# Performance work log

Hardware: AMD Instinct MI355X
Metric: run time of the kernel (lower is better)

The kernel has to match this reference:

```python
import jax, jax.numpy as jnp
import numpy as np

N_NODES = 5000
N_EDGES = 50000
HIDDEN = 64
EDGE_DIM = 16


def setup_inputs() -> dict:
    key = jax.random.key(0)
    ks = jax.random.split(key, 8)
    d = HIDDEN
    h = jax.random.normal(ks[0], (N_NODES, d), dtype=jnp.float32)
    edge_index = jax.random.randint(ks[1], (2, N_EDGES), 0, N_NODES, dtype=jnp.int64)
    edge_features = jax.random.normal(ks[2], (N_EDGES, EDGE_DIM), dtype=jnp.float32)
    # edge-network MLP: Linear(edge_dim, d) -> ReLU -> Linear(d, d*d)
    W1 = jax.random.normal(ks[3], (EDGE_DIM, d), dtype=jnp.float32) * (1.0 / np.sqrt(EDGE_DIM))
    b1 = jnp.zeros((d,), dtype=jnp.float32)
    W2 = jax.random.normal(ks[4], (d, d * d), dtype=jnp.float32) * (1.0 / np.sqrt(d))
    b2 = jnp.zeros((d * d,), dtype=jnp.float32)
    # GRUCell params (torch layout: rows = [reset; update; new])
    W_ih = jax.random.normal(ks[5], (3 * d, d), dtype=jnp.float32) * (1.0 / np.sqrt(d))
    W_hh = jax.random.normal(ks[6], (3 * d, d), dtype=jnp.float32) * (1.0 / np.sqrt(d))
    b_ih = jnp.zeros((3 * d,), dtype=jnp.float32)
    b_hh = jnp.zeros((3 * d,), dtype=jnp.float32)
    return {"h": h, "edge_index": edge_index, "edge_features": edge_features,
            "W1": W1, "b1": b1, "W2": W2, "b2": b2,
            "W_ih": W_ih, "W_hh": W_hh, "b_ih": b_ih, "b_hh": b_hh}


def reference(h, edge_index, edge_features, W1, b1, W2, b2, W_ih, W_hh, b_ih, b_hh):
    n_nodes, d = h.shape
    src, tgt = edge_index[0], edge_index[1]
    # 1) gather sender states
    h_w = h[src]  # (E, d)
    # 2-3) edge MLP -> per-edge transformation matrices (E, d, d)
    A = jax.nn.relu(edge_features @ W1 + b1) @ W2 + b2
    A = A.reshape(-1, d, d)
    # 4) per-edge matvec messages
    msg = jnp.einsum('eij,ej->ei', A, h_w)  # (E, d)
    # 5) scatter-sum aggregation per target node
    m = jax.ops.segment_sum(msg, tgt, num_segments=n_nodes)  # (N, d)
    # 6) GRUCell(m, h) - torch semantics
    gi = m @ W_ih.T + b_ih   # (N, 3d)
    gh = h @ W_hh.T + b_hh   # (N, 3d)
    i_r, i_z, i_n = jnp.split(gi, 3, axis=-1)
    h_r, h_z, h_n = jnp.split(gh, 3, axis=-1)
    r = jax.nn.sigmoid(i_r + h_r)
    z = jax.nn.sigmoid(i_z + h_z)
    n = jnp.tanh(i_n + r * h_n)
    h_new = (1.0 - z) * n + z * h
    return h_new
```

## Files before the change

### kernel.cpp

```cpp
#include <hip/hip_runtime.h>
#include <math.h>

#define N_NODES 5000
#define N_EDGES 50000
#define POISON_I ((int)0xAAAAAAAAu)

typedef _Float16 f16x8 __attribute__((ext_vector_type(8)));
typedef _Float16 f16x4 __attribute__((ext_vector_type(4)));
typedef _Float16 f16x2 __attribute__((ext_vector_type(2)));
typedef float    f32x4 __attribute__((ext_vector_type(4)));

static __device__ __forceinline__ f32x4 mfma16f(f16x8 a, f16x8 b, f32x4 c) {
    return __builtin_amdgcn_mfma_f32_16x16x32_f16(a, b, c, 0, 0, 0);
}
static __device__ __forceinline__ f32x4 mfma16k16(f16x4 a, f16x4 b, f32x4 c) {
    return __builtin_amdgcn_mfma_f32_16x16x16f16(a, b, c, 0, 0, 0);
}

__global__ void prep_kernel(const float* __restrict__ W2, const float* __restrict__ b2,
                            const float* __restrict__ Wih, const float* __restrict__ Whh,
                            const int* __restrict__ ei,
                            _Float16* __restrict__ Br, _Float16* __restrict__ Bg2,
                            int* __restrict__ cnt) {
    int g = blockIdx.x * 256 + threadIdx.x;
    if (g < 33792) {
        int nt = g / 8448, rem = g - nt * 8448;
        int ks = rem >> 6, lane = rem & 63;
        int lo = lane & 15, q = lane >> 4;
        int i = nt * 16 + lo, kap0 = ks * 32 + q * 8;
        f16x8 v;
#pragma unroll
        for (int p = 0; p < 8; ++p) {
            int kap = kap0 + p;
            int k2 = kap >> 7, rem2 = kap & 127;
            int j = rem2 >> 1, k = k2 * 2 + (rem2 & 1);
            float x = 0.f;
            if (k < 64) x = W2[(size_t)k * 4096 + i * 64 + j];
            else if (k == 64) x = b2[i * 64 + j];
            v[p] = (_Float16)x;
        }
        *(f16x8*)(Br + (size_t)g * 8) = v;
        return;
    }
    g -= 33792;
    if (g < 3072) {
        int ct = g >> 7, ks = (g >> 6) & 1, lane = g & 63;
        int lo = lane & 15, q = lane >> 4;
        const float* src = (ct < 12) ? Wih : Whh;
        int r = ((ct < 12) ? ct : ct - 12) * 16 + lo;
        int j0 = ks * 32 + q * 8;
        f16x8 v;
#pragma unroll
        for (int p = 0; p < 8; ++p) v[p] = (_Float16)src[r * 64 + j0 + p];
        *(f16x8*)(Bg2 + (size_t)g * 8) = v;
        return;
    }
    g -= 3072;
    if (g < N_EDGES) atomicAdd(&cnt[ei[N_EDGES + g]], 1);
}

__global__ __launch_bounds__(1024) void scan_kernel(const int* __restrict__ cnt,
                                                    int* __restrict__ off,
                                                    int* __restrict__ cur) {
    __shared__ int s[1024];
    int tid = threadIdx.x;
    int base = tid * 5;
    int loc[5]; int sum = 0;
#pragma unroll
    for (int q = 0; q < 5; ++q) {
        int v = (base + q < N_NODES) ? (cnt[base + q] - POISON_I) : 0;
        loc[q] = sum; sum += v;
    }
    s[tid] = sum; __syncthreads();
    for (int d = 1; d < 1024; d <<= 1) {
        int v = (tid >= d) ? s[tid - d] : 0;
        __syncthreads();
        s[tid] += v;
        __syncthreads();
    }
    int excl = (tid > 0) ? s[tid - 1] : 0;
#pragma unroll
    for (int q = 0; q < 5; ++q)
        if (base + q < N_NODES) { off[base + q] = excl + loc[q]; cur[base + q] = excl + loc[q]; }
    if (tid == 1023) off[N_NODES] = excl + sum;
}

__global__ void scatter_kernel(const int* __restrict__ ei, int* __restrict__ cur,
                               int* __restrict__ srcp, int* __restrict__ eidp) {
    int e = blockIdx.x * 256 + threadIdx.x;
    if (e < N_EDGES) {
        int q = atomicAdd(&cur[ei[N_EDGES + e]], 1);
        srcp[q] = ei[e];
        eidp[q] = e;
    }
}

__global__ __launch_bounds__(1024, 4) void fused_gnn(
    const int* __restrict__ toff, const int* __restrict__ srcp,
    const int* __restrict__ eidp, const float* __restrict__ ef,
    const float* __restrict__ W1, const float* __restrict__ b1,
    const float* __restrict__ h, const _Float16* __restrict__ Br,
    const _Float16* __restrict__ Bg2, const float* __restrict__ bih,
    const float* __restrict__ bhh, float* __restrict__ out)
{
    extern __shared__ __align__(16) char smem[];
    _Float16* tS  = (_Float16*)(smem);
    _Float16* hHi = (_Float16*)(smem + 33280);
    _Float16* hLo = (_Float16*)(smem + 66560);
    int*      nsl = (int*)(smem + 99840);
    _Float16* As    = (_Float16*)(smem);
    float*    mbuf  = (float*)(smem + 33024);
    _Float16* mls   = (_Float16*)(smem + 33024 + 12480);
    _Float16* hls16 = (_Float16*)(smem + 33024 + 14784);
    float*    gbuf  = (float*)(smem + 33024 + 17088);

    int tid = threadIdx.x, w16 = tid >> 6, lane = tid & 63;
    int lo = lane & 15, q = lane >> 4;
    int nt = w16 & 3, kq = w16 >> 2;
    int m0 = blockIdx.x * 16;

    if (tid < 17) {
        int nn = m0 + tid; if (nn > N_NODES) nn = N_NODES;
        nsl[tid] = toff[nn];
    }
    float w1c[16];
#pragma unroll
    for (int k = 0; k < 16; ++k) w1c[k] = W1[k * 64 + lane];
    float b1l = b1[lane];

    f32x4 z4 = {0.f, 0.f, 0.f, 0.f};
    f32x4 acc[4][4];
#pragma unroll
    for (int a = 0; a < 4; ++a)
#pragma unroll
        for (int b = 0; b < 4; ++b) acc[a][b] = z4;
    float sacc = 0.f;
    __syncthreads();

    int nwin = 0;
    {
        int mx = 0;
#pragma unroll
        for (int n = 0; n < 16; ++n) {
            int c = nsl[n + 1] - nsl[n];
            if (c > mx) mx = c;
        }
        nwin = (mx + 15) >> 4;
    }

    for (int ws = 0; ws < nwin; ++ws) {
        if (ws) __syncthreads();
        int epos = ws * 16 + w16;
#pragma unroll 4
        for (int r = 0; r < 16; ++r) {
            int base = nsl[r], cnt2 = nsl[r + 1] - base;
            int cc = r * 16 + w16;
            if (epos < cnt2) {
                int ge = __builtin_amdgcn_readfirstlane(base + epos);
                int src = srcp[ge], eid = eidp[ge];
                float hv = h[(size_t)src * 64 + lane];
                _Float16 hh = (_Float16)hv;
                _Float16 hl = (_Float16)(hv - (float)hh);
                const float* efr = ef + (size_t)eid * 16;
                float tacc = b1l;
#pragma unroll
                for (int k = 0; k < 16; ++k) tacc += efr[k] * w1c[k];
                tS [lane * 260 + cc] = (_Float16)fmaxf(tacc, 0.f);
                hHi[lane * 260 + cc] = hh;
                hLo[lane * 260 + cc] = hl;
            } else {
                tS [lane * 260 + cc] = (_Float16)0.f;
                hHi[lane * 260 + cc] = (_Float16)0.f;
                hLo[lane * 260 + cc] = (_Float16)0.f;
            }
        }
        __syncthreads();
        int cb = w16 * 16 + q * 4;
        f16x4 at[4];
#pragma unroll
        for (int mi = 0; mi < 4; ++mi)
            at[mi] = *(const f16x4*)&tS[(mi * 16 + lo) * 260 + cb];
#pragma unroll
        for (int ni = 0; ni < 4; ++ni) {
            f16x4 bh = *(const f16x4*)&hHi[(ni * 16 + lo) * 260 + cb];
            f16x4 bl = *(const f16x4*)&hLo[(ni * 16 + lo) * 260 + cb];
#pragma unroll
            for (int mi = 0; mi < 4; ++mi) {
                acc[mi][ni] = mfma16k16(at[mi], bh, acc[mi][ni]);
                acc[mi][ni] = mfma16k16(at[mi], bl, acc[mi][ni]);
            }
        }
#pragma unroll
        for (int t4 = 0; t4 < 4; ++t4) {
            f16x4 a4 = *(const f16x4*)&hHi[lane * 260 + w16 * 16 + t4 * 4];
            f16x4 b4 = *(const f16x4*)&hLo[lane * 260 + w16 * 16 + t4 * 4];
#pragma unroll
            for (int i = 0; i < 4; ++i) sacc += (float)a4[i] + (float)b4[i];
        }
    }
    __syncthreads();

    const f16x8* BrV = (const f16x8*)Br;
    f32x4 macc = {0.f, 0.f, 0.f, 0.f};
#pragma unroll
    for (int kc = 0; kc < 4; ++kc) {
        _Float16* aw = As + w16 * 1032;
#pragma unroll
        for (int ni = 0; ni < 4; ++ni)
#pragma unroll
            for (int g0 = 0; g0 < 4; g0 += 2) {
                int k2l = q * 2 + (g0 >> 1);
                f16x2 pv = { (_Float16)acc[kc][ni][g0], (_Float16)acc[kc][ni][g0 + 1] };
                *(f16x2*)(aw + k2l * 128 + (ni * 16 + lo) * 2) = pv;
            }
        __syncthreads();
        const _Float16* Arow = As + lo * 1032 + q * 8;
#pragma unroll
        for (int s = 0; s < 8; ++s) {
            int ksl = kq * 8 + s;
            f16x8 a = *(const f16x8*)(Arow + ksl * 32);
            f16x8 bfr = BrV[(size_t)(nt * 132 + kc * 32 + ksl) * 64 + lane];
            macc = mfma16f(a, bfr, macc);
        }
        __syncthreads();
    }
    {
        f16x2 pv = { (_Float16)sacc, (_Float16)0.f };
        *(f16x2*)(As + w16 * 1032 + lane * 2) = pv;
    }
    __syncthreads();
    {
        f16x8 a = *(const f16x8*)(As + lo * 1032 + kq * 32 + q * 8);
        f16x8 bfr = BrV[(size_t)(nt * 132 + 128 + kq) * 64 + lane];
        macc = mfma16f(a, bfr, macc);
    }
    __syncthreads();
    if (kq > 0) {
#pragma unroll
        for (int g = 0; g < 4; ++g)
            mbuf[(kq - 1) * 1040 + (q * 4 + g) * 65 + nt * 16 + lo] = macc[g];
    }
    if (kq == 3) {
        int t2 = nt * 64 + lane;
#pragma unroll
        for (int r = 0; r < 4; ++r) {
            int e2 = r * 256 + t2, nl = e2 >> 6, j = e2 & 63;
            int n = m0 + nl;
            float hv = (n < N_NODES) ? h[(size_t)n * 64 + j] : 0.f;
            hls16[nl * 72 + j] = (_Float16)hv;
        }
    }
    __syncthreads();
    if (kq == 0) {
#pragma unroll
        for (int g = 0; g < 4; ++g) {
            float mv = macc[g];
#pragma unroll
            for (int pp = 0; pp < 3; ++pp)
                mv += mbuf[pp * 1040 + (q * 4 + g) * 65 + nt * 16 + lo];
            mls[(q * 4 + g) * 72 + nt * 16 + lo] = (_Float16)mv;
        }
    }
    __syncthreads();
    if (w16 < 8) {
        int w8 = w16;
        f16x8 am0 = *(const f16x8*)&mls[lo * 72 + q * 8];
        f16x8 am1 = *(const f16x8*)&mls[lo * 72 + 32 + q * 8];
        f16x8 ah0 = *(const f16x8*)&hls16[lo * 72 + q * 8];
        f16x8 ah1 = *(const f16x8*)&hls16[lo * 72 + 32 + q * 8];
        const f16x8* BgV = (const f16x8*)Bg2;
        f32x4 ga[3] = {z4, z4, z4};
#pragma unroll
        for (int j = 0; j < 3; ++j) {
            int ct = w8 + 8 * j;
            f16x8 bg0 = BgV[(size_t)(ct * 2 + 0) * 64 + lane];
            f16x8 bg1 = BgV[(size_t)(ct * 2 + 1) * 64 + lane];
            f16x8 a0f = (ct < 12) ? am0 : ah0;
            f16x8 a1f = (ct < 12) ? am1 : ah1;
            ga[j] = mfma16f(a0f, bg0, ga[j]);
            ga[j] = mfma16f(a1f, bg1, ga[j]);
        }
#pragma unroll
        for (int j = 0; j < 3; ++j) {
            int ct = w8 + 8 * j;
            int col = (ct < 12) ? (ct * 16 + lo) : (192 + (ct - 12) * 16 + lo);
#pragma unroll
            for (int g = 0; g < 4; ++g) gbuf[(q * 4 + g) * 385 + col] = ga[j][g];
        }
    }
    __syncthreads();
    if (w16 < 8) {
        int i = lane;
#pragma unroll
        for (int u = 0; u < 2; ++u) {
            int nl = w16 * 2 + u, n = m0 + nl;
            if (n >= N_NODES) continue;
            const float* gb = gbuf + nl * 385;
            float ir  = gb[i]       + bih[i];
            float iz  = gb[64 + i]  + bih[64 + i];
            float inn = gb[128 + i] + bih[128 + i];
            float hr  = gb[192 + i] + bhh[i];
            float hz  = gb[256 + i] + bhh[64 + i];
            float hn  = gb[320 + i] + bhh[128 + i];
            float hval = h[(size_t)n * 64 + i];
            float r = 1.f / (1.f + expf(-(ir + hr)));
            float z = 1.f / (1.f + expf(-(iz + hz)));
            float nn = tanhf(inn + r * hn);
            out[n * 64 + i] = (1.f - z) * nn + z * hval;
        }
    }
}

extern "C" void kernel_launch(void* const* d_in, const int* in_sizes, int n_in,
                              void* d_out, int out_size, void* d_ws, size_t ws_size,
                              hipStream_t stream) {
    const float* h   = (const float*)d_in[0];
    const int*   ei  = (const int*)d_in[1];
    const float* ef  = (const float*)d_in[2];
    const float* W1  = (const float*)d_in[3];
    const float* b1  = (const float*)d_in[4];
    const float* W2  = (const float*)d_in[5];
    const float* b2  = (const float*)d_in[6];
    const float* Wih = (const float*)d_in[7];
    const float* Whh = (const float*)d_in[8];
    const float* bih = (const float*)d_in[9];
    const float* bhh = (const float*)d_in[10];
    float* out = (float*)d_out;

    _Float16* Br   = (_Float16*)d_ws;
    _Float16* Bg2  = Br + 270336;
    int*      cnt  = (int*)(Bg2 + 24576);
    int*      toff = cnt + N_NODES;
    int*      cur  = toff + N_NODES + 1;
    int*      srcp = cur + N_NODES;
    int*      eidp = srcp + N_EDGES;

    static bool lds_cfg = false;
    if (!lds_cfg) {
        hipFuncSetAttribute((const void*)fused_gnn,
                            hipFuncAttributeMaxDynamicSharedMemorySize, 99968);
        lds_cfg = true;
    }

    prep_kernel<<<340, 256, 0, stream>>>(W2, b2, Wih, Whh, ei, Br, Bg2, cnt);
    scan_kernel<<<1, 1024, 0, stream>>>(cnt, toff, cur);
    scatter_kernel<<<196, 256, 0, stream>>>(ei, cur, srcp, eidp);
    fused_gnn<<<313, 1024, 99968, stream>>>(toff, srcp, eidp, ef, W1, b1, h,
                                            Br, Bg2, bih, bhh, out);
}
```

Before: 130.5 us.

## Halve fused GNN block to 8 nodes and 512 threads for more blocks

The fused kernel now handles 8 target nodes per block with 8 waves instead of 16 nodes with 16 waves. The grid grows to 625 blocks and LDS per block roughly halves, so more blocks can be resident per CU and the grid fills the device better. Each wave now gathers two edge slots per window, the K-split of the Br matmul goes from four ways to two, and the padded A rows are zero-filled because only 8 nodes are present. The trade-off is that W1, Br and Bg2 are reloaded by twice as many blocks, and per-block sync overhead is amortised over fewer nodes.

```diff
diff --git a/kernel.cpp b/kernel.cpp
--- a/kernel.cpp
+++ b/kernel.cpp
@@ -95,7 +95,7 @@
     }
 }
 
-__global__ __launch_bounds__(1024, 4) void fused_gnn(
+__global__ __launch_bounds__(512) void fused_gnn(
     const int* __restrict__ toff, const int* __restrict__ srcp,
     const int* __restrict__ eidp, const float* __restrict__ ef,
     const float* __restrict__ W1, const float* __restrict__ b1,
@@ -105,23 +105,22 @@
 {
     extern __shared__ __align__(16) char smem[];
     _Float16* tS  = (_Float16*)(smem);
-    _Float16* hHi = (_Float16*)(smem + 33280);
-    _Float16* hLo = (_Float16*)(smem + 66560);
-    int*      nsl = (int*)(smem + 99840);
+    _Float16* hHi = (_Float16*)(smem + 16896);
+    _Float16* hLo = (_Float16*)(smem + 33792);
+    int*      nsl = (int*)(smem + 50688);
     _Float16* As    = (_Float16*)(smem);
-    float*    mbuf  = (float*)(smem + 33024);
-    _Float16* mls   = (_Float16*)(smem + 33024 + 12480);
-    _Float16* hls16 = (_Float16*)(smem + 33024 + 14784);
-    float*    gbuf  = (float*)(smem + 33024 + 17088);
-
-    int tid = threadIdx.x, w16 = tid >> 6, lane = tid & 63;
+    float*    mbuf  = (float*)(smem);
+    _Float16* mls   = (_Float16*)(smem + 4160);
+    _Float16* hls16 = (_Float16*)(smem + 6464);
+    float*    gbuf  = (float*)(smem + 8768);
+
+    int tid = threadIdx.x, w8 = tid >> 6, lane = tid & 63;
     int lo = lane & 15, q = lane >> 4;
-    int nt = w16 & 3, kq = w16 >> 2;
-    int m0 = blockIdx.x * 16;
-
-    if (tid < 17) {
-        int nn = m0 + tid; if (nn > N_NODES) nn = N_NODES;
-        nsl[tid] = toff[nn];
+    int nt = w8 & 3, kq = w8 >> 2;
+    int m0 = blockIdx.x * 8;
+
+    if (tid < 9) {
+        nsl[tid] = toff[m0 + tid];
     }
     float w1c[16];
 #pragma unroll
@@ -137,11 +136,11 @@
     float sacc = 0.f;
     __syncthreads();
 
-    int nwin = 0;
+    int nwin;
     {
         int mx = 0;
 #pragma unroll
-        for (int n = 0; n < 16; ++n) {
+        for (int n = 0; n < 8; ++n) {
             int c = nsl[n + 1] - nsl[n];
             if (c > mx) mx = c;
         }
@@ -150,40 +149,44 @@
 
     for (int ws = 0; ws < nwin; ++ws) {
         if (ws) __syncthreads();
-        int epos = ws * 16 + w16;
-#pragma unroll 4
-        for (int r = 0; r < 16; ++r) {
+        int epos0 = ws * 16;
+#pragma unroll 2
+        for (int r = 0; r < 8; ++r) {
             int base = nsl[r], cnt2 = nsl[r + 1] - base;
-            int cc = r * 16 + w16;
-            if (epos < cnt2) {
-                int ge = __builtin_amdgcn_readfirstlane(base + epos);
-                int src = srcp[ge], eid = eidp[ge];
-                float hv = h[(size_t)src * 64 + lane];
-                _Float16 hh = (_Float16)hv;
-                _Float16 hl = (_Float16)(hv - (float)hh);
-                const float* efr = ef + (size_t)eid * 16;
-                float tacc = b1l;
-#pragma unroll
-                for (int k = 0; k < 16; ++k) tacc += efr[k] * w1c[k];
-                tS [lane * 260 + cc] = (_Float16)fmaxf(tacc, 0.f);
-                hHi[lane * 260 + cc] = hh;
-                hLo[lane * 260 + cc] = hl;
-            } else {
-                tS [lane * 260 + cc] = (_Float16)0.f;
-                hHi[lane * 260 + cc] = (_Float16)0.f;
-                hLo[lane * 260 + cc] = (_Float16)0.f;
+#pragma unroll
+            for (int s2 = 0; s2 < 2; ++s2) {
+                int slot = s2 * 8 + w8;
+                int cc = r * 16 + slot;
+                if (epos0 + slot < cnt2) {
+                    int ge = __builtin_amdgcn_readfirstlane(base + epos0 + slot);
+                    int src = srcp[ge], eid = eidp[ge];
+                    float hv = h[(size_t)src * 64 + lane];
+                    _Float16 hh = (_Float16)hv;
+                    _Float16 hl = (_Float16)(hv - (float)hh);
+                    const float* efr = ef + (size_t)eid * 16;
+                    float tacc = b1l;
+#pragma unroll
+                    for (int k = 0; k < 16; ++k) tacc += efr[k] * w1c[k];
+                    tS [lane * 132 + cc] = (_Float16)fmaxf(tacc, 0.f);
+                    hHi[lane * 132 + cc] = hh;
+                    hLo[lane * 132 + cc] = hl;
+                } else {
+                    tS [lane * 132 + cc] = (_Float16)0.f;
+                    hHi[lane * 132 + cc] = (_Float16)0.f;
+                    hLo[lane * 132 + cc] = (_Float16)0.f;
+                }
             }
         }
         __syncthreads();
-        int cb = w16 * 16 + q * 4;
+        int cb = w8 * 16 + q * 4;
         f16x4 at[4];
 #pragma unroll
         for (int mi = 0; mi < 4; ++mi)
-            at[mi] = *(const f16x4*)&tS[(mi * 16 + lo) * 260 + cb];
+            at[mi] = *(const f16x4*)&tS[(mi * 16 + lo) * 132 + cb];
 #pragma unroll
         for (int ni = 0; ni < 4; ++ni) {
-            f16x4 bh = *(const f16x4*)&hHi[(ni * 16 + lo) * 260 + cb];
-            f16x4 bl = *(const f16x4*)&hLo[(ni * 16 + lo) * 260 + cb];
+            f16x4 bh = *(const f16x4*)&hHi[(ni * 16 + lo) * 132 + cb];
+            f16x4 bl = *(const f16x4*)&hLo[(ni * 16 + lo) * 132 + cb];
 #pragma unroll
             for (int mi = 0; mi < 4; ++mi) {
                 acc[mi][ni] = mfma16k16(at[mi], bh, acc[mi][ni]);
@@ -192,19 +195,25 @@
         }
 #pragma unroll
         for (int t4 = 0; t4 < 4; ++t4) {
-            f16x4 a4 = *(const f16x4*)&hHi[lane * 260 + w16 * 16 + t4 * 4];
-            f16x4 b4 = *(const f16x4*)&hLo[lane * 260 + w16 * 16 + t4 * 4];
+            f16x4 a4 = *(const f16x4*)&hHi[lane * 132 + w8 * 16 + t4 * 4];
+            f16x4 b4 = *(const f16x4*)&hLo[lane * 132 + w8 * 16 + t4 * 4];
 #pragma unroll
             for (int i = 0; i < 4; ++i) sacc += (float)a4[i] + (float)b4[i];
         }
     }
     __syncthreads();
 
+    for (int i = tid; i < 1032; i += 512) {
+        f16x8 zv;
+#pragma unroll
+        for (int p = 0; p < 8; ++p) zv[p] = (_Float16)0.f;
+        *(f16x8*)(As + 8 * 1032 + i * 8) = zv;
+    }
     const f16x8* BrV = (const f16x8*)Br;
     f32x4 macc = {0.f, 0.f, 0.f, 0.f};
 #pragma unroll
     for (int kc = 0; kc < 4; ++kc) {
-        _Float16* aw = As + w16 * 1032;
+        _Float16* aw = As + w8 * 1032;
 #pragma unroll
         for (int ni = 0; ni < 4; ++ni)
 #pragma unroll
@@ -216,8 +225,8 @@
         __syncthreads();
         const _Float16* Arow = As + lo * 1032 + q * 8;
 #pragma unroll
-        for (int s = 0; s < 8; ++s) {
-            int ksl = kq * 8 + s;
+        for (int s = 0; s < 16; ++s) {
+            int ksl = kq * 16 + s;
             f16x8 a = *(const f16x8*)(Arow + ksl * 32);
             f16x8 bfr = BrV[(size_t)(nt * 132 + kc * 32 + ksl) * 64 + lane];
             macc = mfma16f(a, bfr, macc);
@@ -226,27 +235,26 @@
     }
     {
         f16x2 pv = { (_Float16)sacc, (_Float16)0.f };
-        *(f16x2*)(As + w16 * 1032 + lane * 2) = pv;
-    }
-    __syncthreads();
-    {
-        f16x8 a = *(const f16x8*)(As + lo * 1032 + kq * 32 + q * 8);
-        f16x8 bfr = BrV[(size_t)(nt * 132 + 128 + kq) * 64 + lane];
+        *(f16x2*)(As + w8 * 1032 + lane * 2) = pv;
+    }
+    __syncthreads();
+#pragma unroll
+    for (int t = 0; t < 2; ++t) {
+        int ksl = kq * 2 + t;
+        f16x8 a = *(const f16x8*)(As + lo * 1032 + ksl * 32 + q * 8);
+        f16x8 bfr = BrV[(size_t)(nt * 132 + 128 + ksl) * 64 + lane];
         macc = mfma16f(a, bfr, macc);
     }
     __syncthreads();
-    if (kq > 0) {
+    if (kq == 1) {
 #pragma unroll
         for (int g = 0; g < 4; ++g)
-            mbuf[(kq - 1) * 1040 + (q * 4 + g) * 65 + nt * 16 + lo] = macc[g];
-    }
-    if (kq == 3) {
-        int t2 = nt * 64 + lane;
+            mbuf[(q * 4 + g) * 65 + nt * 16 + lo] = macc[g];
+        int t2 = (w8 - 4) * 64 + lane;
 #pragma unroll
         for (int r = 0; r < 4; ++r) {
             int e2 = r * 256 + t2, nl = e2 >> 6, j = e2 & 63;
-            int n = m0 + nl;
-            float hv = (n < N_NODES) ? h[(size_t)n * 64 + j] : 0.f;
+            float hv = (nl < 8) ? h[(size_t)(m0 + nl) * 64 + j] : 0.f;
             hls16[nl * 72 + j] = (_Float16)hv;
         }
     }
@@ -254,16 +262,12 @@
     if (kq == 0) {
 #pragma unroll
         for (int g = 0; g < 4; ++g) {
-            float mv = macc[g];
-#pragma unroll
-            for (int pp = 0; pp < 3; ++pp)
-                mv += mbuf[pp * 1040 + (q * 4 + g) * 65 + nt * 16 + lo];
+            float mv = macc[g] + mbuf[(q * 4 + g) * 65 + nt * 16 + lo];
             mls[(q * 4 + g) * 72 + nt * 16 + lo] = (_Float16)mv;
         }
     }
     __syncthreads();
-    if (w16 < 8) {
-        int w8 = w16;
+    {
         f16x8 am0 = *(const f16x8*)&mls[lo * 72 + q * 8];
         f16x8 am1 = *(const f16x8*)&mls[lo * 72 + 32 + q * 8];
         f16x8 ah0 = *(const f16x8*)&hls16[lo * 72 + q * 8];
@@ -289,25 +293,20 @@
         }
     }
     __syncthreads();
-    if (w16 < 8) {
-        int i = lane;
-#pragma unroll
-        for (int u = 0; u < 2; ++u) {
-            int nl = w16 * 2 + u, n = m0 + nl;
-            if (n >= N_NODES) continue;
-            const float* gb = gbuf + nl * 385;
-            float ir  = gb[i]       + bih[i];
-            float iz  = gb[64 + i]  + bih[64 + i];
-            float inn = gb[128 + i] + bih[128 + i];
-            float hr  = gb[192 + i] + bhh[i];
-            float hz  = gb[256 + i] + bhh[64 + i];
-            float hn  = gb[320 + i] + bhh[128 + i];
-            float hval = h[(size_t)n * 64 + i];
-            float r = 1.f / (1.f + expf(-(ir + hr)));
-            float z = 1.f / (1.f + expf(-(iz + hz)));
-            float nn = tanhf(inn + r * hn);
-            out[n * 64 + i] = (1.f - z) * nn + z * hval;
-        }
+    {
+        int i = lane, nl = w8, n = m0 + nl;
+        const float* gb = gbuf + nl * 385;
+        float ir  = gb[i]       + bih[i];
+        float iz  = gb[64 + i]  + bih[64 + i];
+        float inn = gb[128 + i] + bih[128 + i];
+        float hr  = gb[192 + i] + bhh[i];
+        float hz  = gb[256 + i] + bhh[64 + i];
+        float hn  = gb[320 + i] + bhh[128 + i];
+        float hval = h[(size_t)n * 64 + i];
+        float r = 1.f / (1.f + expf(-(ir + hr)));
+        float z = 1.f / (1.f + expf(-(iz + hz)));
+        float nn = tanhf(inn + r * hn);
+        out[n * 64 + i] = (1.f - z) * nn + z * hval;
     }
 }
 
@@ -338,13 +337,13 @@
     static bool lds_cfg = false;
     if (!lds_cfg) {
         hipFuncSetAttribute((const void*)fused_gnn,
-                            hipFuncAttributeMaxDynamicSharedMemorySize, 99968);
+                            hipFuncAttributeMaxDynamicSharedMemorySize, 51200);
         lds_cfg = true;
     }
 
     prep_kernel<<<340, 256, 0, stream>>>(W2, b2, Wih, Whh, ei, Br, Bg2, cnt);
     scan_kernel<<<1, 1024, 0, stream>>>(cnt, toff, cur);
     scatter_kernel<<<196, 256, 0, stream>>>(ei, cur, srcp, eidp);
-    fused_gnn<<<313, 1024, 99968, stream>>>(toff, srcp, eidp, ef, W1, b1, h,
-                                            Br, Bg2, bih, bhh, out);
-}
+    fused_gnn<<<625, 512, 51200, stream>>>(toff, srcp, eidp, ef, W1, b1, h,
+                                           Br, Bg2, bih, bhh, out);
+}
```

After: 139.8 us. 7.2% more time.

## Move per-edge MLP and gather into CSR-ordered edge stage kernel

Applied to the files above, without the earlier changes.

Replaces the scatter kernel with an edge_stage kernel that computes the first edge-MLP layer and the split-fp16 sender states per edge, writing them to global buffers in target-sorted order. The node kernel then has each wave load its own node's edges directly from global memory into MFMA fragments, with no LDS staging and no max-degree windowing across the 16 nodes of a block. This removes load imbalance from padding to the block's maximum degree and frees LDS for higher occupancy. The cost is an extra global round trip of about 19 MB of fp16 intermediates, plus uncoalesced strided 2-byte fragment loads.

```diff
diff --git a/kernel.cpp b/kernel.cpp
--- a/kernel.cpp
+++ b/kernel.cpp
@@ -21,7 +21,9 @@
                             const float* __restrict__ Wih, const float* __restrict__ Whh,
                             const int* __restrict__ ei,
                             _Float16* __restrict__ Br, _Float16* __restrict__ Bg2,
-                            int* __restrict__ cnt) {
+                            int* __restrict__ cnt,
+                            _Float16* __restrict__ T, _Float16* __restrict__ Hh,
+                            _Float16* __restrict__ Hl) {
     int g = blockIdx.x * 256 + threadIdx.x;
     if (g < 33792) {
         int nt = g / 8448, rem = g - nt * 8448;
@@ -56,7 +58,16 @@
         return;
     }
     g -= 3072;
-    if (g < N_EDGES) atomicAdd(&cnt[ei[N_EDGES + g]], 1);
+    if (g < N_EDGES) {
+        atomicAdd(&cnt[ei[N_EDGES + g]], 1);
+        return;
+    }
+    g -= N_EDGES;
+    if (g < 64) {
+        T [(size_t)N_EDGES * 64 + g] = (_Float16)0.f;
+        Hh[(size_t)N_EDGES * 64 + g] = (_Float16)0.f;
+        Hl[(size_t)N_EDGES * 64 + g] = (_Float16)0.f;
+    }
 }
 
 __global__ __launch_bounds__(1024) void scan_kernel(const int* __restrict__ cnt,
@@ -85,34 +96,45 @@
     if (tid == 1023) off[N_NODES] = excl + sum;
 }
 
-__global__ void scatter_kernel(const int* __restrict__ ei, int* __restrict__ cur,
-                               int* __restrict__ srcp, int* __restrict__ eidp) {
-    int e = blockIdx.x * 256 + threadIdx.x;
-    if (e < N_EDGES) {
-        int q = atomicAdd(&cur[ei[N_EDGES + e]], 1);
-        srcp[q] = ei[e];
-        eidp[q] = e;
-    }
-}
-
-__global__ __launch_bounds__(1024, 4) void fused_gnn(
-    const int* __restrict__ toff, const int* __restrict__ srcp,
-    const int* __restrict__ eidp, const float* __restrict__ ef,
+__global__ __launch_bounds__(256) void edge_stage(
+    const int* __restrict__ ei, const float* __restrict__ ef,
     const float* __restrict__ W1, const float* __restrict__ b1,
-    const float* __restrict__ h, const _Float16* __restrict__ Br,
-    const _Float16* __restrict__ Bg2, const float* __restrict__ bih,
+    const float* __restrict__ h, int* __restrict__ cur,
+    _Float16* __restrict__ T, _Float16* __restrict__ Hh,
+    _Float16* __restrict__ Hl) {
+    int w = threadIdx.x >> 6, lane = threadIdx.x & 63;
+    int e = blockIdx.x * 4 + w;
+    int src = ei[e], tgt = ei[N_EDGES + e];
+    int q;
+    if (lane == 0) q = atomicAdd(&cur[tgt], 1);
+    q = __shfl(q, 0);
+    float hv = h[(size_t)src * 64 + lane];
+    _Float16 hh = (_Float16)hv;
+    _Float16 hl = (_Float16)(hv - (float)hh);
+    const float* efr = ef + (size_t)e * 16;
+    float tacc = b1[lane];
+#pragma unroll
+    for (int k = 0; k < 16; ++k) tacc += efr[k] * W1[k * 64 + lane];
+    T [(size_t)q * 64 + lane] = (_Float16)fmaxf(tacc, 0.f);
+    Hh[(size_t)q * 64 + lane] = hh;
+    Hl[(size_t)q * 64 + lane] = hl;
+}
+
+__global__ __launch_bounds__(1024) void node_gnn(
+    const int* __restrict__ toff, const _Float16* __restrict__ T,
+    const _Float16* __restrict__ Hh, const _Float16* __restrict__ Hl,
+    const _Float16* __restrict__ Br, const _Float16* __restrict__ Bg2,
+    const float* __restrict__ h, const float* __restrict__ bih,
     const float* __restrict__ bhh, float* __restrict__ out)
 {
     extern __shared__ __align__(16) char smem[];
-    _Float16* tS  = (_Float16*)(smem);
-    _Float16* hHi = (_Float16*)(smem + 33280);
-    _Float16* hLo = (_Float16*)(smem + 66560);
-    int*      nsl = (int*)(smem + 99840);
-    _Float16* As    = (_Float16*)(smem);
-    float*    mbuf  = (float*)(smem + 33024);
-    _Float16* mls   = (_Float16*)(smem + 33024 + 12480);
-    _Float16* hls16 = (_Float16*)(smem + 33024 + 14784);
-    float*    gbuf  = (float*)(smem + 33024 + 17088);
+    _Float16* As   = (_Float16*)smem;
+    float*    mbuf  = (float*)smem;
+    _Float16* mls   = (_Float16*)(smem + 12480);
+    _Float16* hls16 = (_Float16*)(smem + 14784);
+    float*    gbuf  = (float*)(smem + 33024);
+    float*    Svec  = (float*)(smem + 57664);
+    int*      nsl   = (int*)(smem + 61760);
 
     int tid = threadIdx.x, w16 = tid >> 6, lane = tid & 63;
     int lo = lane & 15, q = lane >> 4;
@@ -123,10 +145,8 @@
         int nn = m0 + tid; if (nn > N_NODES) nn = N_NODES;
         nsl[tid] = toff[nn];
     }
-    float w1c[16];
-#pragma unroll
-    for (int k = 0; k < 16; ++k) w1c[k] = W1[k * 64 + lane];
-    float b1l = b1[lane];
+    __syncthreads();
+    int base = nsl[w16], deg = nsl[w16 + 1] - base;
 
     f32x4 z4 = {0.f, 0.f, 0.f, 0.f};
     f32x4 acc[4][4];
@@ -134,71 +154,52 @@
     for (int a = 0; a < 4; ++a)
 #pragma unroll
         for (int b = 0; b < 4; ++b) acc[a][b] = z4;
-    float sacc = 0.f;
-    __syncthreads();
-
-    int nwin = 0;
-    {
-        int mx = 0;
-#pragma unroll
-        for (int n = 0; n < 16; ++n) {
-            int c = nsl[n + 1] - nsl[n];
-            if (c > mx) mx = c;
-        }
-        nwin = (mx + 15) >> 4;
-    }
-
-    for (int ws = 0; ws < nwin; ++ws) {
-        if (ws) __syncthreads();
-        int epos = ws * 16 + w16;
-#pragma unroll 4
-        for (int r = 0; r < 16; ++r) {
-            int base = nsl[r], cnt2 = nsl[r + 1] - base;
-            int cc = r * 16 + w16;
-            if (epos < cnt2) {
-                int ge = __builtin_amdgcn_readfirstlane(base + epos);
-                int src = srcp[ge], eid = eidp[ge];
-                float hv = h[(size_t)src * 64 + lane];
-                _Float16 hh = (_Float16)hv;
-                _Float16 hl = (_Float16)(hv - (float)hh);
-                const float* efr = ef + (size_t)eid * 16;
-                float tacc = b1l;
-#pragma unroll
-                for (int k = 0; k < 16; ++k) tacc += efr[k] * w1c[k];
-                tS [lane * 260 + cc] = (_Float16)fmaxf(tacc, 0.f);
-                hHi[lane * 260 + cc] = hh;
-                hLo[lane * 260 + cc] = hl;
-            } else {
-                tS [lane * 260 + cc] = (_Float16)0.f;
-                hHi[lane * 260 + cc] = (_Float16)0.f;
-                hLo[lane * 260 + cc] = (_Float16)0.f;
+    float sp[4] = {0.f, 0.f, 0.f, 0.f};
+
+    int nw = (deg + 15) >> 4;
+    for (int ws = 0; ws < nw; ++ws) {
+        int ri[4];
+#pragma unroll
+        for (int k = 0; k < 4; ++k) {
+            int s = ws * 16 + q * 4 + k;
+            ri[k] = (s < deg) ? (base + s) : N_EDGES;
+        }
+        f16x4 at[4], bh[4], bl[4];
+#pragma unroll
+        for (int mi = 0; mi < 4; ++mi)
+#pragma unroll
+            for (int k = 0; k < 4; ++k)
+                at[mi][k] = T[(size_t)ri[k] * 64 + mi * 16 + lo];
+#pragma unroll
+        for (int ni = 0; ni < 4; ++ni)
+#pragma unroll
+            for (int k = 0; k < 4; ++k) {
+                bh[ni][k] = Hh[(size_t)ri[k] * 64 + ni * 16 + lo];
+                bl[ni][k] = Hl[(size_t)ri[k] * 64 + ni * 16 + lo];
             }
-        }
-        __syncthreads();
-        int cb = w16 * 16 + q * 4;
-        f16x4 at[4];
-#pragma unroll
-        for (int mi = 0; mi < 4; ++mi)
-            at[mi] = *(const f16x4*)&tS[(mi * 16 + lo) * 260 + cb];
+#pragma unroll
+        for (int ni = 0; ni < 4; ++ni)
+#pragma unroll
+            for (int mi = 0; mi < 4; ++mi) {
+                acc[mi][ni] = mfma16k16(at[mi], bh[ni], acc[mi][ni]);
+                acc[mi][ni] = mfma16k16(at[mi], bl[ni], acc[mi][ni]);
+            }
 #pragma unroll
         for (int ni = 0; ni < 4; ++ni) {
-            f16x4 bh = *(const f16x4*)&hHi[(ni * 16 + lo) * 260 + cb];
-            f16x4 bl = *(const f16x4*)&hLo[(ni * 16 + lo) * 260 + cb];
-#pragma unroll
-            for (int mi = 0; mi < 4; ++mi) {
-                acc[mi][ni] = mfma16k16(at[mi], bh, acc[mi][ni]);
-                acc[mi][ni] = mfma16k16(at[mi], bl, acc[mi][ni]);
-            }
-        }
-#pragma unroll
-        for (int t4 = 0; t4 < 4; ++t4) {
-            f16x4 a4 = *(const f16x4*)&hHi[lane * 260 + w16 * 16 + t4 * 4];
-            f16x4 b4 = *(const f16x4*)&hLo[lane * 260 + w16 * 16 + t4 * 4];
-#pragma unroll
-            for (int i = 0; i < 4; ++i) sacc += (float)a4[i] + (float)b4[i];
-        }
-    }
-    __syncthreads();
+            float s4 = 0.f;
+#pragma unroll
+            for (int k = 0; k < 4; ++k)
+                s4 += (float)bh[ni][k] + (float)bl[ni][k];
+            sp[ni] += s4;
+        }
+    }
+#pragma unroll
+    for (int ni = 0; ni < 4; ++ni) {
+        float v = sp[ni];
+        v += __shfl_xor(v, 16);
+        v += __shfl_xor(v, 32);
+        if (q == 0) Svec[w16 * 64 + ni * 16 + lo] = v;
+    }
 
     const f16x8* BrV = (const f16x8*)Br;
     f32x4 macc = {0.f, 0.f, 0.f, 0.f};
@@ -225,6 +226,7 @@
         __syncthreads();
     }
     {
+        float sacc = Svec[w16 * 64 + lane];
         f16x2 pv = { (_Float16)sacc, (_Float16)0.f };
         *(f16x2*)(As + w16 * 1032 + lane * 2) = pv;
     }
@@ -327,24 +329,26 @@
     const float* bhh = (const float*)d_in[10];
     float* out = (float*)d_out;
 
-    _Float16* Br   = (_Float16*)d_ws;
+    _Float16* T    = (_Float16*)d_ws;
+    _Float16* Hh   = T + (size_t)(N_EDGES + 1) * 64;
+    _Float16* Hl   = Hh + (size_t)(N_EDGES + 1) * 64;
+    _Float16* Br   = Hl + (size_t)(N_EDGES + 1) * 64;
     _Float16* Bg2  = Br + 270336;
     int*      cnt  = (int*)(Bg2 + 24576);
     int*      toff = cnt + N_NODES;
     int*      cur  = toff + N_NODES + 1;
-    int*      srcp = cur + N_NODES;
-    int*      eidp = srcp + N_EDGES;
 
     static bool lds_cfg = false;
     if (!lds_cfg) {
-        hipFuncSetAttribute((const void*)fused_gnn,
-                            hipFuncAttributeMaxDynamicSharedMemorySize, 99968);
+        hipFuncSetAttribute((const void*)node_gnn,
+                            hipFuncAttributeMaxDynamicSharedMemorySize, 61952);
         lds_cfg = true;
     }
 
-    prep_kernel<<<340, 256, 0, stream>>>(W2, b2, Wih, Whh, ei, Br, Bg2, cnt);
+    prep_kernel<<<340, 256, 0, stream>>>(W2, b2, Wih, Whh, ei, Br, Bg2, cnt,
+                                         T, Hh, Hl);
     scan_kernel<<<1, 1024, 0, stream>>>(cnt, toff, cur);
-    scatter_kernel<<<196, 256, 0, stream>>>(ei, cur, srcp, eidp);
-    fused_gnn<<<313, 1024, 99968, stream>>>(toff, srcp, eidp, ef, W1, b1, h,
-                                            Br, Bg2, bih, bhh, out);
-}
+    edge_stage<<<12500, 256, 0, stream>>>(ei, ef, W1, b1, h, cur, T, Hh, Hl);
+    node_gnn<<<313, 1024, 61952, stream>>>(toff, T, Hh, Hl, Br, Bg2, h,
+                                           bih, bhh, out);
+}
```

Result: slower. 136.4 us (+4.6%).
